# Performance work log

Measured on AMD Instinct MI355X. Metric: run time of the kernel, lower is better.

The kernel has to match this reference:

```python
import jax, jax.numpy as jnp
import numpy as np

TOP_K = 2  # k in TopKGate


def setup_inputs() -> dict:
    key = jax.random.key(0)
    k1, k2, k3 = jax.random.split(key, 3)
    B, S, H, E = 4, 2048, 1024, 8
    hidden_states = jax.random.normal(k1, (B, S, H), dtype=jnp.float32)
    Wg = jax.random.normal(k2, (H, E), dtype=jnp.float32) * (H ** -0.5)
    We = jax.random.normal(k3, (E, H, H), dtype=jnp.float32) * (H ** -0.5)
    be = jnp.zeros((E, H), dtype=jnp.float32)
    return {"hidden_states": hidden_states, "Wg": Wg, "We": We, "be": be}


def reference(hidden_states, Wg, We, be):
    # hidden_states: [B, S, H]; Wg: [H, E]; We: [E, H, H]; be: [E, H]
    B, S, H = hidden_states.shape
    T = B * S
    x = hidden_states.reshape(T, H)

    # TopKGate: linear gate -> softmax -> top-k -> renormalize combine weights
    probs = jax.nn.softmax(x @ Wg, axis=-1)              # [T, E]
    top_vals, top_idx = jax.lax.top_k(probs, TOP_K)     # [T, K]
    gates = top_vals / jnp.sum(top_vals, axis=-1, keepdims=True)

    # Experts: run each token through each expert Linear, then gather top-k
    expert_out = jnp.einsum('th,ehd->etd', x, We) + be[:, None, :]  # [E, T, H]
    tok = jnp.arange(T)[:, None]                         # [T, 1]
    sel = expert_out[top_idx, tok, :]                    # [T, K, H]

    # Weighted combine over top-k experts
    out = jnp.sum(gates[..., None] * sel, axis=1)        # [T, H]
    return out.reshape(B, S, H)
```

## Files before the change

### kernel.cpp

```cpp
#include <hip/hip_runtime.h>
#include <hip/hip_bf16.h>

#define H 1024
#define NEXP 8
#define T_TOK 8192
#define CAP 8192
#define TM 128
#define TN 128
#define TPB 16
#define CNTSTRIDE 32
#define NTRANS 2048

typedef __bf16 bf16x8 __attribute__((ext_vector_type(8)));
typedef __bf16 bf16x4 __attribute__((ext_vector_type(4)));
typedef float f32x4 __attribute__((ext_vector_type(4)));

__device__ __forceinline__ void async16(void* lds, const void* g) {
    __builtin_amdgcn_global_load_lds(
        (const __attribute__((address_space(1))) void*)g,
        (__attribute__((address_space(3))) void*)lds, 16, 0, 0);
}

__global__ __launch_bounds__(256) void moe_prep(
    const float* __restrict__ We, __bf16* __restrict__ WeT,
    const float* __restrict__ x, const float* __restrict__ Wg,
    __bf16* __restrict__ Xb, int* __restrict__ cnt,
    int* __restrict__ ltok, float* __restrict__ lgate,
    int* __restrict__ tsel, float* __restrict__ tgate) {
    __shared__ __align__(16) char smem[64 * 65 * 4];
    const int tid = threadIdx.x;

    if (blockIdx.x < NTRANS) {
        float (*t)[65] = (float(*)[65])smem;
        const int tt = blockIdx.x;
        const int e  = tt >> 8;
        const int d0 = ((tt >> 4) & 15) * 64;
        const int h0 = (tt & 15) * 64;
        const int tx = tid & 15;
        const int ty = tid >> 4;
        const float* src = We + ((size_t)e << 20);
        __bf16* dst = WeT + ((size_t)e << 20);
#pragma unroll
        for (int p = 0; p < 4; ++p) {
            const int row = p * 16 + ty;
            const float4 v = *(const float4*)(src + (size_t)(h0 + row) * H + d0 + tx * 4);
            t[row][tx * 4 + 0] = v.x; t[row][tx * 4 + 1] = v.y;
            t[row][tx * 4 + 2] = v.z; t[row][tx * 4 + 3] = v.w;
        }
        __syncthreads();
#pragma unroll
        for (int p = 0; p < 4; ++p) {
            const int drow = p * 16 + ty;
            bf16x4 o;
            o[0] = (__bf16)t[tx * 4 + 0][drow];
            o[1] = (__bf16)t[tx * 4 + 1][drow];
            o[2] = (__bf16)t[tx * 4 + 2][drow];
            o[3] = (__bf16)t[tx * 4 + 3][drow];
            *(bf16x4*)(dst + (size_t)(d0 + drow) * H + h0 + tx * 4) = o;
        }
        return;
    }

    int*   sE    = (int*)smem;
    float* sG    = (float*)(smem + 128);
    int*   lcnt  = (int*)(smem + 256);
    int*   lbase = (int*)(smem + 288);
    int*   lslot = (int*)(smem + 320);
    const int lane = tid & 63;
    const int wave = tid >> 6;
    const int base = (blockIdx.x - NTRANS) * TPB;

    float a[4][NEXP];
#pragma unroll
    for (int tl4 = 0; tl4 < 4; ++tl4)
#pragma unroll
        for (int e = 0; e < NEXP; ++e) a[tl4][e] = 0.f;

#pragma unroll
    for (int j = 0; j < H / 256; ++j) {
        const int h = j * 256 + lane * 4;
        float4 wg0[4], wg1[4];
#pragma unroll
        for (int c = 0; c < 4; ++c) {
            wg0[c] = *(const float4*)(Wg + (h + c) * NEXP);
            wg1[c] = *(const float4*)(Wg + (h + c) * NEXP + 4);
        }
#pragma unroll
        for (int tl4 = 0; tl4 < 4; ++tl4) {
            const int t = base + wave * 4 + tl4;
            const float4 xv = *(const float4*)(x + (size_t)t * H + h);
            bf16x4 xo;
            xo[0] = (__bf16)xv.x; xo[1] = (__bf16)xv.y;
            xo[2] = (__bf16)xv.z; xo[3] = (__bf16)xv.w;
            *(bf16x4*)(Xb + (size_t)t * H + h) = xo;
            const float xc[4] = {xv.x, xv.y, xv.z, xv.w};
#pragma unroll
            for (int c = 0; c < 4; ++c) {
                a[tl4][0] += xc[c] * wg0[c].x; a[tl4][1] += xc[c] * wg0[c].y;
                a[tl4][2] += xc[c] * wg0[c].z; a[tl4][3] += xc[c] * wg0[c].w;
                a[tl4][4] += xc[c] * wg1[c].x; a[tl4][5] += xc[c] * wg1[c].y;
                a[tl4][6] += xc[c] * wg1[c].z; a[tl4][7] += xc[c] * wg1[c].w;
            }
        }
    }

#pragma unroll
    for (int tl4 = 0; tl4 < 4; ++tl4) {
        const int tl = wave * 4 + tl4;
#pragma unroll
        for (int e = 0; e < NEXP; ++e) {
#pragma unroll
            for (int off = 32; off > 0; off >>= 1)
                a[tl4][e] += __shfl_xor(a[tl4][e], off, 64);
        }
        int i0 = 0;
#pragma unroll
        for (int e = 1; e < NEXP; ++e) if (a[tl4][e] > a[tl4][i0]) i0 = e;
        int i1 = (i0 == 0) ? 1 : 0;
#pragma unroll
        for (int e = 0; e < NEXP; ++e) if (e != i0 && a[tl4][e] > a[tl4][i1]) i1 = e;
        const float ex = __expf(a[tl4][i1] - a[tl4][i0]);
        const float g0 = 1.f / (1.f + ex);
        const float g1 = ex / (1.f + ex);
        if (lane == 0) {
            sE[tl * 2] = i0; sE[tl * 2 + 1] = i1;
            sG[tl * 2] = g0; sG[tl * 2 + 1] = g1;
        }
    }
    if (tid < NEXP) lcnt[tid] = 0;
    __syncthreads();
    if (tid < TPB * 2) lslot[tid] = atomicAdd(&lcnt[sE[tid]], 1);
    __syncthreads();
    if (tid < NEXP) lbase[tid] = lcnt[tid] ? atomicAdd(&cnt[tid * CNTSTRIDE], lcnt[tid]) : 0;
    __syncthreads();
    if (tid < TPB * 2) {
        const int e = sE[tid];
        const int s = lbase[e] + lslot[tid];
        const int t = base + (tid >> 1);
        ltok[e * CAP + s]  = t;
        lgate[e * CAP + s] = sG[tid];
        tsel[t * 2 + (tid & 1)]  = e * CAP + s;
        tgate[t * 2 + (tid & 1)] = sG[tid];
    }
}

__global__ __launch_bounds__(256) void moe_gemm(
    const __bf16* __restrict__ Xb, const __bf16* __restrict__ WeT,
    const float* __restrict__ be, const int* __restrict__ cnt,
    const int* __restrict__ ltok, const float* __restrict__ lgate,
    __bf16* __restrict__ Eout) {
    const int e  = blockIdx.x & 7;
    const int nt = (blockIdx.x >> 3) & 7;
    const int mt = blockIdx.x >> 6;
    const int ne = cnt[e * CNTSTRIDE];
    const int m0 = mt * TM;
    if (m0 >= ne) return;
    const int n0 = nt * TN;
    int off = 0;
    for (int i2 = 0; i2 < e; ++i2) off += cnt[i2 * CNTSTRIDE];

    __shared__ __align__(16) __bf16 smem[4 * 4096];
    __bf16* Al  = smem;
    __bf16* Al2 = smem + 4096;
    __bf16* Bl  = smem + 8192;
    __bf16* Bl2 = smem + 12288;
    __shared__ int tokL[TM];

    const int tid = threadIdx.x;
    const int lane = tid & 63;
    const int wave = tid >> 6;

    if (tid < TM) {
        const int gi = m0 + tid;
        tokL[tid] = (gi < ne) ? ltok[e * CAP + gi] : 0;
    }
    __syncthreads();

    const __bf16* Bt = WeT + ((size_t)e << 20);
    const int qr = lane >> 4;
    const int rr = lane & 15;
    const int wr = (wave >> 1) * 64;
    const int wc = (wave & 1) * 64;

    f32x4 acc[4][4];
    const f32x4 z = {0.f, 0.f, 0.f, 0.f};
#pragma unroll
    for (int i = 0; i < 4; ++i)
#pragma unroll
        for (int j = 0; j < 4; ++j) acc[i][j] = z;

    const int c0 = tid, c1 = tid + 256;
    const int ar0 = c0 >> 2, ak0 = (((c0 & 3) ^ ((c0 >> 3) & 3)) * 8);
    const int ar1 = c1 >> 2, ak1 = (((c1 & 3) ^ ((c1 >> 3) & 3)) * 8);
    const size_t arow0 = (size_t)tokL[ar0] * H;
    const size_t arow1 = (size_t)tokL[ar1] * H;
    const size_t brow0 = (size_t)(n0 + ar0) * H;
    const size_t brow1 = (size_t)(n0 + ar1) * H;

    for (int k0 = 0; k0 < H; k0 += 64) {
        async16(&Al [c0 * 8], Xb + arow0 + k0 + ak0);
        async16(&Al [c1 * 8], Xb + arow1 + k0 + ak1);
        async16(&Al2[c0 * 8], Xb + arow0 + k0 + 32 + ak0);
        async16(&Al2[c1 * 8], Xb + arow1 + k0 + 32 + ak1);
        async16(&Bl [c0 * 8], Bt + brow0 + k0 + ak0);
        async16(&Bl [c1 * 8], Bt + brow1 + k0 + ak1);
        async16(&Bl2[c0 * 8], Bt + brow0 + k0 + 32 + ak0);
        async16(&Bl2[c1 * 8], Bt + brow1 + k0 + 32 + ak1);
        __syncthreads();
        {
            bf16x8 af[4], bfr[4];
#pragma unroll
            for (int i = 0; i < 4; ++i) {
                const int ra = wr + i * 16 + rr;
                af[i] = *(const bf16x8*)&Al[ra * 32 + ((qr ^ ((ra >> 1) & 3)) * 8)];
            }
#pragma unroll
            for (int j = 0; j < 4; ++j) {
                const int rb = wc + j * 16 + rr;
                bfr[j] = *(const bf16x8*)&Bl[rb * 32 + ((qr ^ ((rb >> 1) & 3)) * 8)];
            }
#pragma unroll
            for (int i = 0; i < 4; ++i)
#pragma unroll
                for (int j = 0; j < 4; ++j)
                    acc[i][j] = __builtin_amdgcn_mfma_f32_16x16x32_bf16(af[i], bfr[j], acc[i][j], 0, 0, 0);
        }
        {
            bf16x8 af[4], bfr[4];
#pragma unroll
            for (int i = 0; i < 4; ++i) {
                const int ra = wr + i * 16 + rr;
                af[i] = *(const bf16x8*)&Al2[ra * 32 + ((qr ^ ((ra >> 1) & 3)) * 8)];
            }
#pragma unroll
            for (int j = 0; j < 4; ++j) {
                const int rb = wc + j * 16 + rr;
                bfr[j] = *(const bf16x8*)&Bl2[rb * 32 + ((qr ^ ((rb >> 1) & 3)) * 8)];
            }
#pragma unroll
            for (int i = 0; i < 4; ++i)
#pragma unroll
                for (int j = 0; j < 4; ++j)
                    acc[i][j] = __builtin_amdgcn_mfma_f32_16x16x32_bf16(af[i], bfr[j], acc[i][j], 0, 0, 0);
        }
        __syncthreads();
    }

    float bev[4];
#pragma unroll
    for (int j = 0; j < 4; ++j) bev[j] = be[e * H + n0 + wc + j * 16 + rr];

    __bf16* Cw = smem + wave * 4096;
#pragma unroll
    for (int i = 0; i < 4; ++i) {
#pragma unroll
        for (int reg = 0; reg < 4; ++reg) {
            const int row = i * 16 + qr * 4 + reg;
            const int key = (row & 7) * 8;
#pragma unroll
            for (int j = 0; j < 4; ++j) {
                const int c = j * 16 + rr;
                Cw[row * 64 + (c ^ key)] = (__bf16)(acc[i][j][reg] + bev[j]);
            }
        }
    }
    const int lrr = lane & 7, lrg = lane >> 3;
#pragma unroll
    for (int p = 0; p < 8; ++p) {
        const int row = p * 8 + lrg;
        const int rglob = m0 + wr + row;
        if (rglob < ne) {
            const int idx8 = ((lrr ^ (row & 7)) * 8);
            const bf16x8 v = *(const bf16x8*)&Cw[row * 64 + idx8];
            *(bf16x8*)(Eout + (size_t)(off + rglob) * H + n0 + wc + lrr * 8) = v;
        }
    }
}

__global__ __launch_bounds__(256) void moe_combine(
    const __bf16* __restrict__ Eout, const int* __restrict__ cnt,
    const int* __restrict__ tsel, const float* __restrict__ tgate,
    float* __restrict__ out) {
    __shared__ int offs[NEXP];
    if (threadIdx.x < NEXP) {
        int o = 0;
        for (int i = 0; i < (int)threadIdx.x; ++i) o += cnt[i * CNTSTRIDE];
        offs[threadIdx.x] = o;
    }
    __syncthreads();
    const int wave = threadIdx.x >> 6, lane = threadIdx.x & 63;
    const int t = blockIdx.x * 4 + wave;
    const int sel0 = tsel[t * 2],  sel1 = tsel[t * 2 + 1];
    const float g0 = tgate[t * 2], g1  = tgate[t * 2 + 1];
    const int e0 = sel0 >> 13, s0 = sel0 & (CAP - 1);
    const int e1 = sel1 >> 13, s1 = sel1 & (CAP - 1);
    const __bf16* r0 = Eout + (size_t)(offs[e0] + s0) * H;
    const __bf16* r1 = Eout + (size_t)(offs[e1] + s1) * H;
    float* orow = out + (size_t)t * H;
#pragma unroll
    for (int c = 0; c < 2; ++c) {
        const int d = c * 512 + lane * 8;
        const bf16x8 a = *(const bf16x8*)(r0 + d);
        const bf16x8 b = *(const bf16x8*)(r1 + d);
        float4 o0, o1;
        o0.x = g0 * (float)a[0] + g1 * (float)b[0];
        o0.y = g0 * (float)a[1] + g1 * (float)b[1];
        o0.z = g0 * (float)a[2] + g1 * (float)b[2];
        o0.w = g0 * (float)a[3] + g1 * (float)b[3];
        o1.x = g0 * (float)a[4] + g1 * (float)b[4];
        o1.y = g0 * (float)a[5] + g1 * (float)b[5];
        o1.z = g0 * (float)a[6] + g1 * (float)b[6];
        o1.w = g0 * (float)a[7] + g1 * (float)b[7];
        *(float4*)(orow + d)     = o0;
        *(float4*)(orow + d + 4) = o1;
    }
}

extern "C" void kernel_launch(void* const* d_in, const int* in_sizes, int n_in,
                              void* d_out, int out_size, void* d_ws, size_t ws_size,
                              hipStream_t stream) {
    const float* x  = (const float*)d_in[0];
    const float* Wg = (const float*)d_in[1];
    const float* We = (const float*)d_in[2];
    const float* be = (const float*)d_in[3];
    float* out = (float*)d_out;

    char* ws = (char*)d_ws;
    __bf16* Xb   = (__bf16*)ws;
    __bf16* WeT  = (__bf16*)(ws + ((size_t)16 << 20));
    __bf16* Eout = (__bf16*)(ws + ((size_t)32 << 20));
    char*   meta = ws + ((size_t)64 << 20);
    int*    cnt  = (int*)meta;
    int*    ltok = (int*)(meta + 1024);
    float*  lgat = (float*)(meta + 1024 + (size_t)NEXP * CAP * 4);
    int*    tsel = (int*)(meta + 1024 + (size_t)NEXP * CAP * 8);
    float*  tgat = (float*)(meta + 1024 + (size_t)NEXP * CAP * 8 + (size_t)T_TOK * 8);

    hipMemsetAsync(cnt, 0, NEXP * CNTSTRIDE * sizeof(int), stream);

    moe_prep<<<NTRANS + T_TOK / TPB, 256, 0, stream>>>(We, WeT, x, Wg, Xb, cnt,
                                                       ltok, lgat, tsel, tgat);
    moe_gemm<<<8 * 8 * (T_TOK / TM), 256, 0, stream>>>(Xb, WeT, be, cnt, ltok, lgat, Eout);
    moe_combine<<<T_TOK / 4, 256, 0, stream>>>(Eout, cnt, tsel, tgat, out);
}
```

Measured before the change: 203.1 us.

## Interleave transpose and gating blocks, one token per wave, wider bf16 stores

The prep kernel now alternates weight-transpose blocks and gating blocks by block parity instead of running all transpose blocks first, so memory-bound and compute-bound work mix across the GPU. Gating now handles 4 tokens per block, one per wave, which gives 2048 gating blocks with fewer registers each. The transpose write-back uses 16-byte bf16x8 stores instead of 8-byte stores. The unused lgate buffer is removed from prep and gemm. Smaller gating blocks mean more blocks and more global atomics on the expert counters.

```diff
diff --git a/kernel.cpp b/kernel.cpp
--- a/kernel.cpp
+++ b/kernel.cpp
@@ -7,9 +7,8 @@
 #define CAP 8192
 #define TM 128
 #define TN 128
-#define TPB 16
 #define CNTSTRIDE 32
-#define NTRANS 2048
+#define NPREP 4096
 
 typedef __bf16 bf16x8 __attribute__((ext_vector_type(8)));
 typedef __bf16 bf16x4 __attribute__((ext_vector_type(4)));
@@ -25,14 +24,14 @@
     const float* __restrict__ We, __bf16* __restrict__ WeT,
     const float* __restrict__ x, const float* __restrict__ Wg,
     __bf16* __restrict__ Xb, int* __restrict__ cnt,
-    int* __restrict__ ltok, float* __restrict__ lgate,
+    int* __restrict__ ltok,
     int* __restrict__ tsel, float* __restrict__ tgate) {
     __shared__ __align__(16) char smem[64 * 65 * 4];
     const int tid = threadIdx.x;
 
-    if (blockIdx.x < NTRANS) {
+    if ((blockIdx.x & 1) == 0) {
         float (*t)[65] = (float(*)[65])smem;
-        const int tt = blockIdx.x;
+        const int tt = blockIdx.x >> 1;
         const int e  = tt >> 8;
         const int d0 = ((tt >> 4) & 15) * 64;
         const int h0 = (tt & 15) * 64;
@@ -49,105 +48,101 @@
         }
         __syncthreads();
 #pragma unroll
-        for (int p = 0; p < 4; ++p) {
-            const int drow = p * 16 + ty;
-            bf16x4 o;
-            o[0] = (__bf16)t[tx * 4 + 0][drow];
-            o[1] = (__bf16)t[tx * 4 + 1][drow];
-            o[2] = (__bf16)t[tx * 4 + 2][drow];
-            o[3] = (__bf16)t[tx * 4 + 3][drow];
-            *(bf16x4*)(dst + (size_t)(d0 + drow) * H + h0 + tx * 4) = o;
+        for (int qq = 0; qq < 2; ++qq) {
+            const int q = tid + qq * 256;
+            const int drow = q >> 3;
+            const int seg  = q & 7;
+            bf16x8 o;
+#pragma unroll
+            for (int i = 0; i < 8; ++i) o[i] = (__bf16)t[seg * 8 + i][drow];
+            *(bf16x8*)(dst + (size_t)(d0 + drow) * H + h0 + seg * 8) = o;
         }
         return;
     }
 
     int*   sE    = (int*)smem;
-    float* sG    = (float*)(smem + 128);
-    int*   lcnt  = (int*)(smem + 256);
-    int*   lbase = (int*)(smem + 288);
-    int*   lslot = (int*)(smem + 320);
+    float* sG    = (float*)(smem + 64);
+    int*   lcnt  = (int*)(smem + 128);
+    int*   lbase = (int*)(smem + 160);
+    int*   lslot = (int*)(smem + 192);
     const int lane = tid & 63;
     const int wave = tid >> 6;
-    const int base = (blockIdx.x - NTRANS) * TPB;
-
-    float a[4][NEXP];
-#pragma unroll
-    for (int tl4 = 0; tl4 < 4; ++tl4)
-#pragma unroll
-        for (int e = 0; e < NEXP; ++e) a[tl4][e] = 0.f;
-
-#pragma unroll
-    for (int j = 0; j < H / 256; ++j) {
-        const int h = j * 256 + lane * 4;
-        float4 wg0[4], wg1[4];
-#pragma unroll
-        for (int c = 0; c < 4; ++c) {
-            wg0[c] = *(const float4*)(Wg + (h + c) * NEXP);
-            wg1[c] = *(const float4*)(Wg + (h + c) * NEXP + 4);
-        }
-#pragma unroll
-        for (int tl4 = 0; tl4 < 4; ++tl4) {
-            const int t = base + wave * 4 + tl4;
-            const float4 xv = *(const float4*)(x + (size_t)t * H + h);
-            bf16x4 xo;
-            xo[0] = (__bf16)xv.x; xo[1] = (__bf16)xv.y;
-            xo[2] = (__bf16)xv.z; xo[3] = (__bf16)xv.w;
-            *(bf16x4*)(Xb + (size_t)t * H + h) = xo;
-            const float xc[4] = {xv.x, xv.y, xv.z, xv.w};
-#pragma unroll
-            for (int c = 0; c < 4; ++c) {
-                a[tl4][0] += xc[c] * wg0[c].x; a[tl4][1] += xc[c] * wg0[c].y;
-                a[tl4][2] += xc[c] * wg0[c].z; a[tl4][3] += xc[c] * wg0[c].w;
-                a[tl4][4] += xc[c] * wg1[c].x; a[tl4][5] += xc[c] * wg1[c].y;
-                a[tl4][6] += xc[c] * wg1[c].z; a[tl4][7] += xc[c] * wg1[c].w;
-            }
-        }
-    }
-
-#pragma unroll
-    for (int tl4 = 0; tl4 < 4; ++tl4) {
-        const int tl = wave * 4 + tl4;
-#pragma unroll
-        for (int e = 0; e < NEXP; ++e) {
-#pragma unroll
-            for (int off = 32; off > 0; off >>= 1)
-                a[tl4][e] += __shfl_xor(a[tl4][e], off, 64);
-        }
-        int i0 = 0;
-#pragma unroll
-        for (int e = 1; e < NEXP; ++e) if (a[tl4][e] > a[tl4][i0]) i0 = e;
-        int i1 = (i0 == 0) ? 1 : 0;
-#pragma unroll
-        for (int e = 0; e < NEXP; ++e) if (e != i0 && a[tl4][e] > a[tl4][i1]) i1 = e;
-        const float ex = __expf(a[tl4][i1] - a[tl4][i0]);
-        const float g0 = 1.f / (1.f + ex);
-        const float g1 = ex / (1.f + ex);
-        if (lane == 0) {
-            sE[tl * 2] = i0; sE[tl * 2 + 1] = i1;
-            sG[tl * 2] = g0; sG[tl * 2 + 1] = g1;
-        }
+    const int base = (blockIdx.x >> 1) * 4;
+    const int t = base + wave;
+
+    const float* xr  = x  + (size_t)t * H;
+    __bf16*      xbr = Xb + (size_t)t * H;
+
+    const float4 xv0 = *(const float4*)(xr + 0   + lane * 4);
+    const float4 xv1 = *(const float4*)(xr + 256 + lane * 4);
+    const float4 xv2 = *(const float4*)(xr + 512 + lane * 4);
+    const float4 xv3 = *(const float4*)(xr + 768 + lane * 4);
+    const float4 xv[4] = {xv0, xv1, xv2, xv3};
+
+    float a[NEXP];
+#pragma unroll
+    for (int e = 0; e < NEXP; ++e) a[e] = 0.f;
+
+#pragma unroll
+    for (int c = 0; c < 4; ++c) {
+        const int h = c * 256 + lane * 4;
+        bf16x4 xo;
+        xo[0] = (__bf16)xv[c].x; xo[1] = (__bf16)xv[c].y;
+        xo[2] = (__bf16)xv[c].z; xo[3] = (__bf16)xv[c].w;
+        *(bf16x4*)(xbr + h) = xo;
+        const float* wgp = Wg + (size_t)h * NEXP;
+        float4 w[8];
+#pragma unroll
+        for (int r2 = 0; r2 < 8; ++r2) w[r2] = *(const float4*)(wgp + r2 * 4);
+        const float xc[4] = {xv[c].x, xv[c].y, xv[c].z, xv[c].w};
+#pragma unroll
+        for (int i = 0; i < 4; ++i) {
+            a[0] += xc[i] * w[i * 2].x; a[1] += xc[i] * w[i * 2].y;
+            a[2] += xc[i] * w[i * 2].z; a[3] += xc[i] * w[i * 2].w;
+            a[4] += xc[i] * w[i * 2 + 1].x; a[5] += xc[i] * w[i * 2 + 1].y;
+            a[6] += xc[i] * w[i * 2 + 1].z; a[7] += xc[i] * w[i * 2 + 1].w;
+        }
+    }
+
+#pragma unroll
+    for (int e = 0; e < NEXP; ++e) {
+#pragma unroll
+        for (int off = 32; off > 0; off >>= 1)
+            a[e] += __shfl_xor(a[e], off, 64);
+    }
+    int i0 = 0;
+#pragma unroll
+    for (int e = 1; e < NEXP; ++e) if (a[e] > a[i0]) i0 = e;
+    int i1 = (i0 == 0) ? 1 : 0;
+#pragma unroll
+    for (int e = 0; e < NEXP; ++e) if (e != i0 && a[e] > a[i1]) i1 = e;
+    const float ex = __expf(a[i1] - a[i0]);
+    const float g0 = 1.f / (1.f + ex);
+    const float g1 = ex / (1.f + ex);
+    if (lane == 0) {
+        sE[wave * 2] = i0; sE[wave * 2 + 1] = i1;
+        sG[wave * 2] = g0; sG[wave * 2 + 1] = g1;
     }
     if (tid < NEXP) lcnt[tid] = 0;
     __syncthreads();
-    if (tid < TPB * 2) lslot[tid] = atomicAdd(&lcnt[sE[tid]], 1);
+    if (tid < 8) lslot[tid] = atomicAdd(&lcnt[sE[tid]], 1);
     __syncthreads();
     if (tid < NEXP) lbase[tid] = lcnt[tid] ? atomicAdd(&cnt[tid * CNTSTRIDE], lcnt[tid]) : 0;
     __syncthreads();
-    if (tid < TPB * 2) {
+    if (tid < 8) {
         const int e = sE[tid];
         const int s = lbase[e] + lslot[tid];
-        const int t = base + (tid >> 1);
-        ltok[e * CAP + s]  = t;
-        lgate[e * CAP + s] = sG[tid];
-        tsel[t * 2 + (tid & 1)]  = e * CAP + s;
-        tgate[t * 2 + (tid & 1)] = sG[tid];
+        const int tt2 = base + (tid >> 1);
+        ltok[e * CAP + s] = tt2;
+        tsel[tt2 * 2 + (tid & 1)]  = e * CAP + s;
+        tgate[tt2 * 2 + (tid & 1)] = sG[tid];
     }
 }
 
 __global__ __launch_bounds__(256) void moe_gemm(
     const __bf16* __restrict__ Xb, const __bf16* __restrict__ WeT,
     const float* __restrict__ be, const int* __restrict__ cnt,
-    const int* __restrict__ ltok, const float* __restrict__ lgate,
+    const int* __restrict__ ltok,
     __bf16* __restrict__ Eout) {
     const int e  = blockIdx.x & 7;
     const int nt = (blockIdx.x >> 3) & 7;
@@ -332,14 +327,12 @@
     char*   meta = ws + ((size_t)64 << 20);
     int*    cnt  = (int*)meta;
     int*    ltok = (int*)(meta + 1024);
-    float*  lgat = (float*)(meta + 1024 + (size_t)NEXP * CAP * 4);
     int*    tsel = (int*)(meta + 1024 + (size_t)NEXP * CAP * 8);
     float*  tgat = (float*)(meta + 1024 + (size_t)NEXP * CAP * 8 + (size_t)T_TOK * 8);
 
     hipMemsetAsync(cnt, 0, NEXP * CNTSTRIDE * sizeof(int), stream);
 
-    moe_prep<<<NTRANS + T_TOK / TPB, 256, 0, stream>>>(We, WeT, x, Wg, Xb, cnt,
-                                                       ltok, lgat, tsel, tgat);
-    moe_gemm<<<8 * 8 * (T_TOK / TM), 256, 0, stream>>>(Xb, WeT, be, cnt, ltok, lgat, Eout);
+    moe_prep<<<NPREP, 256, 0, stream>>>(We, WeT, x, Wg, Xb, cnt, ltok, tsel, tgat);
+    moe_gemm<<<8 * 8 * (T_TOK / TM), 256, 0, stream>>>(Xb, WeT, be, cnt, ltok, Eout);
     moe_combine<<<T_TOK / 4, 256, 0, stream>>>(Eout, cnt, tsel, tgat, out);
 }
```

Result: slower. 226.8 us (+11.7%).
